# Kernel optimization log

Measured on AMD Instinct MI355X. Metric: run time of the kernel, lower is better.

## Reference

```python
import jax, jax.numpy as jnp
import numpy as np

N_NODES = 50000
N_EDGES = 800000
IN_DIM, HID, OUT = 128, 64, 64
NUM_REL = 2
LN_EPS = 1e-5


def setup_inputs() -> dict:
    key = jax.random.key(0)
    ks = jax.random.split(key, 16)
    inp = {
        "x": jax.random.normal(ks[0], (N_NODES, IN_DIM), dtype=jnp.float32),
        "edge_index": jax.random.randint(ks[1], (2, N_EDGES), 0, N_NODES, dtype=jnp.int64),
        "edge_type": jax.random.randint(ks[2], (N_EDGES,), 0, NUM_REL, dtype=jnp.int64),
        # layer 1 params (RGCNConv input->hidden + LayerNorm)
        "W1": jax.random.normal(ks[3], (NUM_REL, IN_DIM, HID), dtype=jnp.float32) * 0.05,
        "root1": jax.random.normal(ks[4], (IN_DIM, HID), dtype=jnp.float32) * 0.05,
        "b1": jnp.zeros((HID,), dtype=jnp.float32),
        "g1": jnp.ones((HID,), dtype=jnp.float32),
        "beta1": jnp.zeros((HID,), dtype=jnp.float32),
        # layer 2 params (RGCNConv hidden->output + LayerNorm)
        "W2": jax.random.normal(ks[5], (NUM_REL, HID, OUT), dtype=jnp.float32) * 0.05,
        "root2": jax.random.normal(ks[6], (HID, OUT), dtype=jnp.float32) * 0.05,
        "b2": jnp.zeros((OUT,), dtype=jnp.float32),
        "g2": jnp.ones((OUT,), dtype=jnp.float32),
        "beta2": jnp.zeros((OUT,), dtype=jnp.float32),
    }
    return inp


def rgcn_conv(x, W, root, bias, src, dst, edge_type, num_nodes):
    # PyG RGCNConv (aggr='mean'): out = x @ root + bias + sum_r mean_{j in N_r(i)} x_j @ W_r
    out = x @ root + bias
    for r in range(NUM_REL):
        mask = (edge_type == r).astype(x.dtype)        # [E]
        proj = x @ W[r]                                 # [N, out]
        msg = proj[src] * mask[:, None]                 # [E, out] gather + mask
        agg = jax.ops.segment_sum(msg, dst, num_segments=num_nodes)   # scatter-add
        cnt = jax.ops.segment_sum(mask, dst, num_segments=num_nodes)  # per-relation in-degree
        out = out + agg / jnp.maximum(cnt, 1.0)[:, None]
    return out


def layer_norm(x, g, b):
    mu = jnp.mean(x, axis=-1, keepdims=True)
    var = jnp.mean(jnp.square(x - mu), axis=-1, keepdims=True)
    return (x - mu) * jax.lax.rsqrt(var + LN_EPS) * g + b


def reference(x, edge_index, edge_type, W1, root1, b1, g1, beta1, W2, root2, b2, g2, beta2):
    src, dst = edge_index[0], edge_index[1]
    h = rgcn_conv(x, W1, root1, b1, src, dst, edge_type, x.shape[0])
    h = layer_norm(h, g1, beta1)
    h = jax.nn.gelu(h, approximate=False)  # dropout is identity in eval mode
    h = rgcn_conv(h, W2, root2, b2, src, dst, edge_type, x.shape[0])
    h = layer_norm(h, g2, beta2)
    return h
```

## Files before the change

kernel.cpp:

```cpp
#include <hip/hip_runtime.h>
#include <hip/hip_bf16.h>
#include <math.h>

#define IN_DIM 128
#define HID 64
#define NREL 2

using f32x4 = __attribute__((ext_vector_type(4))) float;
using s16x8 = __attribute__((ext_vector_type(8))) short;

__device__ __forceinline__ short f2bf(float f) {
    unsigned u = __float_as_uint(f);
    unsigned r = (u + 0x7fffu + ((u >> 16) & 1u)) >> 16;
    return (short)r;
}
__device__ __forceinline__ float bf2f(short b) {
    return __uint_as_float(((unsigned)(unsigned short)b) << 16);
}

__global__ void zero_ints(int* p, int n) {
    int i = blockIdx.x * blockDim.x + threadIdx.x;
    if (i < n) p[i] = 0;
}

__global__ void count_edges(const int* __restrict__ et, const int* __restrict__ dst,
                            int* __restrict__ cnt, int E, int N) {
    int e = blockIdx.x * blockDim.x + threadIdx.x;
    if (e < E) {
        atomicAdd(&cnt[et[e] * N + dst[e]], 1);
    }
}

#define SCAN_T 256
#define SCAN_I 4
__global__ void scan_phase1(const int* __restrict__ in, int* __restrict__ excl,
                            int* __restrict__ bsum, int n) {
    __shared__ int sdata[SCAN_T];
    int b = blockIdx.x;
    int t = threadIdx.x;
    int base = b * SCAN_T * SCAN_I;
    int v[SCAN_I];
    int s = 0;
#pragma unroll
    for (int i = 0; i < SCAN_I; ++i) {
        int idx = base + t * SCAN_I + i;
        v[i] = (idx < n) ? in[idx] : 0;
        s += v[i];
    }
    sdata[t] = s;
    __syncthreads();
    for (int off = 1; off < SCAN_T; off <<= 1) {
        int x = (t >= off) ? sdata[t - off] : 0;
        __syncthreads();
        sdata[t] += x;
        __syncthreads();
    }
    int run = sdata[t] - s;
    if (bsum && t == SCAN_T - 1) bsum[b] = sdata[SCAN_T - 1];
#pragma unroll
    for (int i = 0; i < SCAN_I; ++i) {
        int idx = base + t * SCAN_I + i;
        if (idx < n) excl[idx] = run;
        run += v[i];
    }
}

__global__ void scan_phase3(const int* __restrict__ excl, const int* __restrict__ boff,
                            int* __restrict__ rowptr, int* __restrict__ cursor,
                            int n, int total) {
    int i = blockIdx.x * blockDim.x + threadIdx.x;
    if (i < n) {
        int v = excl[i] + boff[i / (SCAN_T * SCAN_I)];
        rowptr[i] = v;
        cursor[i] = v;
    }
    if (i == 0) rowptr[n] = total;
}

__global__ void fill_edges(const int* __restrict__ et, const int* __restrict__ src,
                           const int* __restrict__ dst, int* __restrict__ cursor,
                           int* __restrict__ col, int E, int N) {
    int e = blockIdx.x * blockDim.x + threadIdx.x;
    if (e < E) {
        int slot = atomicAdd(&cursor[et[e] * N + dst[e]], 1);
        col[slot] = src[e];
    }
}

__device__ __forceinline__ void repack_one(const float* Wa, const float* Wb,
                                           const float* Wr, short* Wf, int T,
                                           int idx) {
    int g = idx >> 9;
    int r = idx & 511;
    int lane = r >> 3;
    int j = r & 7;
    int part = g & 1;
    int ct = g >> 1;
    int t = ct % T;
    int c = ct / T;
    int col = c * 16 + (lane & 15);
    int k = t * 32 + ((lane >> 4) << 3) + j;
    const float* Wg = (col < 64) ? Wa : (col < 128) ? Wb : Wr;
    float v = Wg[(size_t)k * 64 + (col & 63)];
    short hi = f2bf(v);
    Wf[idx] = part ? f2bf(v - bf2f(hi)) : hi;
}

__global__ void repack_w_frag(const float* __restrict__ W1,
                              const float* __restrict__ root1,
                              const float* __restrict__ W2,
                              const float* __restrict__ root2,
                              short* __restrict__ Wf1, short* __restrict__ Wf2) {
    const int L1 = 12 * 4 * 2 * 512;
    const int L2 = 12 * 2 * 2 * 512;
    int tid = blockIdx.x * blockDim.x + threadIdx.x;
    if (tid < L1) {
        repack_one(W1, W1 + (size_t)IN_DIM * 64, root1, Wf1, 4, tid);
    } else if (tid < L1 + L2) {
        repack_one(W2, W2 + (size_t)HID * 64, root2, Wf2, 2, tid - L1);
    }
}

template <int K>
__global__ __launch_bounds__(256) void gemm_mfma(
    const float* __restrict__ X, const short* __restrict__ Wf,
    float* __restrict__ PA, float* __restrict__ PB, float* __restrict__ PR,
    int M) {
    constexpr int T = K / 32;
    const int lane = threadIdx.x & 63;
    const int row0 = (blockIdx.x * 4 + (threadIdx.x >> 6)) * 16;

    int arow = row0 + (lane & 15);
    if (arow > M - 1) arow = M - 1;
    const float* xr = X + (size_t)arow * K + ((lane >> 4) << 3);
    const s16x8* WfV = (const s16x8*)Wf;

    f32x4 acc[12];
#pragma unroll
    for (int c = 0; c < 12; ++c) acc[c] = (f32x4){0.f, 0.f, 0.f, 0.f};

#pragma unroll
    for (int t = 0; t < T; ++t) {
        const float4 a0 = *reinterpret_cast<const float4*>(xr + t * 32);
        const float4 a1 = *reinterpret_cast<const float4*>(xr + t * 32 + 4);
        const float av[8] = {a0.x, a0.y, a0.z, a0.w, a1.x, a1.y, a1.z, a1.w};
        s16x8 ah, al;
#pragma unroll
        for (int j = 0; j < 8; ++j) {
            short h = f2bf(av[j]);
            ah[j] = h;
            al[j] = f2bf(av[j] - bf2f(h));
        }
#pragma unroll
        for (int c = 0; c < 12; ++c) {
            s16x8 bh = WfV[(size_t)((c * T + t) * 2 + 0) * 64 + lane];
            s16x8 bl = WfV[(size_t)((c * T + t) * 2 + 1) * 64 + lane];
            acc[c] = __builtin_amdgcn_mfma_f32_16x16x32_bf16(ah, bh, acc[c], 0, 0, 0);
            acc[c] = __builtin_amdgcn_mfma_f32_16x16x32_bf16(al, bh, acc[c], 0, 0, 0);
            acc[c] = __builtin_amdgcn_mfma_f32_16x16x32_bf16(ah, bl, acc[c], 0, 0, 0);
        }
    }

    const int drow = row0 + ((lane >> 4) << 2);
    const int dcol = lane & 15;
#pragma unroll
    for (int c = 0; c < 12; ++c) {
        float* base = (c < 4) ? PA : (c < 8) ? PB : PR;
        const int cc = (c & 3) * 16 + dcol;
#pragma unroll
        for (int q = 0; q < 4; ++q) {
            const int row = drow + q;
            if (row < M) base[(size_t)row * 64 + cc] = acc[c][q];
        }
    }
}

__device__ __forceinline__ float4 shfl_xor_f4(float4 v, int m) {
    return make_float4(__shfl_xor(v.x, m), __shfl_xor(v.y, m),
                       __shfl_xor(v.z, m), __shfl_xor(v.w, m));
}

__global__ __launch_bounds__(256) void agg_ln_kernel(
    const float* __restrict__ PA, const float* __restrict__ PB,
    const float* __restrict__ PR,
    const int* __restrict__ rowptr, const int* __restrict__ col,
    const float* __restrict__ bias, const float* __restrict__ g,
    const float* __restrict__ beta,
    float* __restrict__ out, int N, int gelu) {
    const int t = threadIdx.x;
    const int lane = t & 63;
    const int sub = lane >> 4;
    const int c = lane & 15;
    const int node = blockIdx.x * 4 + (t >> 6);
    if (node >= N) return;

    float4 acc = *reinterpret_cast<const float4*>(PR + (size_t)node * 64 + c * 4);
    {
        float4 b4 = *reinterpret_cast<const float4*>(bias + c * 4);
        acc.x += b4.x; acc.y += b4.y; acc.z += b4.z; acc.w += b4.w;
    }

#pragma unroll
    for (int r = 0; r < 2; ++r) {
        const float* __restrict__ P = r ? PB : PA;
        const int beg = rowptr[r * N + node];
        const int end = rowptr[r * N + node + 1];
        float4 s0 = make_float4(0.f, 0.f, 0.f, 0.f);
        float4 s1 = make_float4(0.f, 0.f, 0.f, 0.f);
        for (int i = beg + sub; i < end; i += 8) {
            const float4 v0 =
                *reinterpret_cast<const float4*>(P + (size_t)col[i] * 64 + c * 4);
            s0.x += v0.x; s0.y += v0.y; s0.z += v0.z; s0.w += v0.w;
            const int j = i + 4;
            if (j < end) {
                const float4 v1 =
                    *reinterpret_cast<const float4*>(P + (size_t)col[j] * 64 + c * 4);
                s1.x += v1.x; s1.y += v1.y; s1.z += v1.z; s1.w += v1.w;
            }
        }
        s0.x += s1.x; s0.y += s1.y; s0.z += s1.z; s0.w += s1.w;
        float4 o = shfl_xor_f4(s0, 16);
        s0.x += o.x; s0.y += o.y; s0.z += o.z; s0.w += o.w;
        o = shfl_xor_f4(s0, 32);
        s0.x += o.x; s0.y += o.y; s0.z += o.z; s0.w += o.w;
        const int deg = end - beg;
        if (deg > 0) {
            const float inv = 1.f / (float)deg;
            acc.x += s0.x * inv; acc.y += s0.y * inv;
            acc.z += s0.z * inv; acc.w += s0.w * inv;
        }
    }

    float ps = acc.x + acc.y + acc.z + acc.w;
#pragma unroll
    for (int off = 1; off <= 8; off <<= 1) ps += __shfl_xor(ps, off);
    const float mu = ps * (1.f / 64.f);
    const float4 d = make_float4(acc.x - mu, acc.y - mu, acc.z - mu, acc.w - mu);
    float vs = d.x * d.x + d.y * d.y + d.z * d.z + d.w * d.w;
#pragma unroll
    for (int off = 1; off <= 8; off <<= 1) vs += __shfl_xor(vs, off);
    const float rstd = 1.f / sqrtf(vs * (1.f / 64.f) + 1e-5f);

    const float4 g4 = *reinterpret_cast<const float4*>(g + c * 4);
    const float4 be4 = *reinterpret_cast<const float4*>(beta + c * 4);
    float4 y;
    y.x = d.x * rstd * g4.x + be4.x;
    y.y = d.y * rstd * g4.y + be4.y;
    y.z = d.z * rstd * g4.z + be4.z;
    y.w = d.w * rstd * g4.w + be4.w;

    if (gelu) {
        y.x = 0.5f * y.x * (1.f + erff(y.x * 0.70710678118654752440f));
        y.y = 0.5f * y.y * (1.f + erff(y.y * 0.70710678118654752440f));
        y.z = 0.5f * y.z * (1.f + erff(y.z * 0.70710678118654752440f));
        y.w = 0.5f * y.w * (1.f + erff(y.w * 0.70710678118654752440f));
    }

    if (sub == 0)
        *reinterpret_cast<float4*>(out + (size_t)node * 64 + c * 4) = y;
}

extern "C" void kernel_launch(void* const* d_in, const int* in_sizes, int n_in,
                              void* d_out, int out_size, void* d_ws, size_t ws_size,
                              hipStream_t stream) {
    const float* x = (const float*)d_in[0];
    const int* ei = (const int*)d_in[1];
    const int* et = (const int*)d_in[2];
    const float* W1 = (const float*)d_in[3];
    const float* root1 = (const float*)d_in[4];
    const float* b1 = (const float*)d_in[5];
    const float* g1 = (const float*)d_in[6];
    const float* beta1 = (const float*)d_in[7];
    const float* W2 = (const float*)d_in[8];
    const float* root2 = (const float*)d_in[9];
    const float* b2 = (const float*)d_in[10];
    const float* g2 = (const float*)d_in[11];
    const float* beta2 = (const float*)d_in[12];

    const int E = in_sizes[2];
    const int N = in_sizes[0] / IN_DIM;
    const int nseg = NREL * N;

    const int WF1 = 12 * 4 * 2 * 512;
    const int WF2 = 12 * 2 * 2 * 512;

    short* Wf1 = (short*)d_ws;
    short* Wf2 = Wf1 + WF1;
    float* PA = (float*)(Wf2 + WF2);
    float* PB = PA + (size_t)N * 64;
    float* PR = PB + (size_t)N * 64;
    float* H  = PR + (size_t)N * 64;
    int* cnt    = (int*)(H + (size_t)N * 64);
    int* excl   = cnt + nseg;
    int* rowptr = excl + nseg;
    int* cursor = rowptr + nseg + 1;
    int* colA   = cursor + nseg;
    int* bsum   = colA + E;
    int* boff   = bsum + 256;

    const int* esrc = ei;
    const int* edst = ei + E;

    zero_ints<<<(nseg + 255) / 256, 256, 0, stream>>>(cnt, nseg);
    count_edges<<<(E + 255) / 256, 256, 0, stream>>>(et, edst, cnt, E, N);
    int nb = (nseg + SCAN_T * SCAN_I - 1) / (SCAN_T * SCAN_I);
    scan_phase1<<<nb, SCAN_T, 0, stream>>>(cnt, excl, bsum, nseg);
    scan_phase1<<<1, SCAN_T, 0, stream>>>(bsum, boff, nullptr, nb);
    scan_phase3<<<(nseg + 255) / 256, 256, 0, stream>>>(excl, boff, rowptr, cursor,
                                                        nseg, E);
    fill_edges<<<(E + 255) / 256, 256, 0, stream>>>(et, esrc, edst, cursor, colA, E, N);

    repack_w_frag<<<(WF1 + WF2 + 255) / 256, 256, 0, stream>>>(
        W1, root1, W2, root2, Wf1, Wf2);

    int gblocks = (N + 63) / 64;
    gemm_mfma<IN_DIM><<<gblocks, 256, 0, stream>>>(x, Wf1, PA, PB, PR, N);
    agg_ln_kernel<<<(N + 3) / 4, 256, 0, stream>>>(PA, PB, PR, rowptr, colA, b1, g1,
                                                   beta1, H, N, 1);

    gemm_mfma<HID><<<gblocks, 256, 0, stream>>>(H, Wf2, PA, PB, PR, N);
    agg_ln_kernel<<<(N + 3) / 4, 256, 0, stream>>>(PA, PB, PR, rowptr, colA, b2, g2,
                                                   beta2, (float*)d_out, N, 0);
}
```

Before: 327.2 us.

## Split GEMM output columns across wave pairs and software-pipeline weight fragment loads

Each wave now computes 6 of the 12 16-column output tiles for a 16-row strip, with two waves sharing a row strip, so each block covers 32 rows and the grid doubles. A-operand loads and bf16 hi/lo splits are hoisted ahead of the MFMA loop, and B fragments are double-buffered, with the next column group loaded while the current one runs its MFMAs. This cuts accumulator registers and raises parallelism and latency hiding in the projection GEMMs. In exchange, each X row is loaded and converted twice, once per wave in the pair.

```diff
diff --git a/kernel.cpp b/kernel.cpp
--- a/kernel.cpp
+++ b/kernel.cpp
@@ -128,49 +128,86 @@
     int M) {
     constexpr int T = K / 32;
     const int lane = threadIdx.x & 63;
-    const int row0 = (blockIdx.x * 4 + (threadIdx.x >> 6)) * 16;
+    const int wid = threadIdx.x >> 6;
+    const int row0 = blockIdx.x * 32 + (wid >> 1) * 16;
+    const int cbase = (wid & 1) * 6;
 
     int arow = row0 + (lane & 15);
     if (arow > M - 1) arow = M - 1;
     const float* xr = X + (size_t)arow * K + ((lane >> 4) << 3);
     const s16x8* WfV = (const s16x8*)Wf;
 
-    f32x4 acc[12];
-#pragma unroll
-    for (int c = 0; c < 12; ++c) acc[c] = (f32x4){0.f, 0.f, 0.f, 0.f};
-
+    float4 xa[T][2];
 #pragma unroll
     for (int t = 0; t < T; ++t) {
-        const float4 a0 = *reinterpret_cast<const float4*>(xr + t * 32);
-        const float4 a1 = *reinterpret_cast<const float4*>(xr + t * 32 + 4);
-        const float av[8] = {a0.x, a0.y, a0.z, a0.w, a1.x, a1.y, a1.z, a1.w};
-        s16x8 ah, al;
+        xa[t][0] = *reinterpret_cast<const float4*>(xr + t * 32);
+        xa[t][1] = *reinterpret_cast<const float4*>(xr + t * 32 + 4);
+    }
+    s16x8 ah[T], al[T];
+#pragma unroll
+    for (int t = 0; t < T; ++t) {
+        const float av[8] = {xa[t][0].x, xa[t][0].y, xa[t][0].z, xa[t][0].w,
+                             xa[t][1].x, xa[t][1].y, xa[t][1].z, xa[t][1].w};
 #pragma unroll
         for (int j = 0; j < 8; ++j) {
             short h = f2bf(av[j]);
-            ah[j] = h;
-            al[j] = f2bf(av[j] - bf2f(h));
+            ah[t][j] = h;
+            al[t][j] = f2bf(av[j] - bf2f(h));
         }
-#pragma unroll
-        for (int c = 0; c < 12; ++c) {
-            s16x8 bh = WfV[(size_t)((c * T + t) * 2 + 0) * 64 + lane];
-            s16x8 bl = WfV[(size_t)((c * T + t) * 2 + 1) * 64 + lane];
-            acc[c] = __builtin_amdgcn_mfma_f32_16x16x32_bf16(ah, bh, acc[c], 0, 0, 0);
-            acc[c] = __builtin_amdgcn_mfma_f32_16x16x32_bf16(al, bh, acc[c], 0, 0, 0);
-            acc[c] = __builtin_amdgcn_mfma_f32_16x16x32_bf16(ah, bl, acc[c], 0, 0, 0);
-        }
-    }
+    }
+
+    f32x4 acc[6];
+#pragma unroll
+    for (int c = 0; c < 6; ++c) acc[c] = (f32x4){0.f, 0.f, 0.f, 0.f};
+
+    s16x8 bhA[T], blA[T], bhB[T], blB[T];
+
+#define LOADB(H, L, CG)                                                       \
+    {                                                                         \
+        _Pragma("unroll") for (int t = 0; t < T; ++t) {                       \
+            H[t] = WfV[(size_t)(((CG) * T + t) * 2 + 0) * 64 + lane];         \
+            L[t] = WfV[(size_t)(((CG) * T + t) * 2 + 1) * 64 + lane];         \
+        }                                                                     \
+    }
+#define DOMFMA(H, L, CI)                                                      \
+    {                                                                         \
+        _Pragma("unroll") for (int t = 0; t < T; ++t) {                       \
+            acc[CI] = __builtin_amdgcn_mfma_f32_16x16x32_bf16(ah[t], H[t],    \
+                                                              acc[CI], 0, 0, 0); \
+            acc[CI] = __builtin_amdgcn_mfma_f32_16x16x32_bf16(al[t], H[t],    \
+                                                              acc[CI], 0, 0, 0); \
+            acc[CI] = __builtin_amdgcn_mfma_f32_16x16x32_bf16(ah[t], L[t],    \
+                                                              acc[CI], 0, 0, 0); \
+        }                                                                     \
+    }
+
+    LOADB(bhA, blA, cbase + 0);
+    LOADB(bhB, blB, cbase + 1);
+    DOMFMA(bhA, blA, 0);
+    LOADB(bhA, blA, cbase + 2);
+    DOMFMA(bhB, blB, 1);
+    LOADB(bhB, blB, cbase + 3);
+    DOMFMA(bhA, blA, 2);
+    LOADB(bhA, blA, cbase + 4);
+    DOMFMA(bhB, blB, 3);
+    LOADB(bhB, blB, cbase + 5);
+    DOMFMA(bhA, blA, 4);
+    DOMFMA(bhB, blB, 5);
+
+#undef LOADB
+#undef DOMFMA
 
     const int drow = row0 + ((lane >> 4) << 2);
     const int dcol = lane & 15;
 #pragma unroll
-    for (int c = 0; c < 12; ++c) {
-        float* base = (c < 4) ? PA : (c < 8) ? PB : PR;
-        const int cc = (c & 3) * 16 + dcol;
+    for (int ci = 0; ci < 6; ++ci) {
+        const int cg = cbase + ci;
+        float* base = (cg < 4) ? PA : (cg < 8) ? PB : PR;
+        const int cc = (cg & 3) * 16 + dcol;
 #pragma unroll
         for (int q = 0; q < 4; ++q) {
             const int row = drow + q;
-            if (row < M) base[(size_t)row * 64 + cc] = acc[c][q];
+            if (row < M) base[(size_t)row * 64 + cc] = acc[ci][q];
         }
     }
 }
@@ -313,7 +350,7 @@
     repack_w_frag<<<(WF1 + WF2 + 255) / 256, 256, 0, stream>>>(
         W1, root1, W2, root2, Wf1, Wf2);
 
-    int gblocks = (N + 63) / 64;
+    int gblocks = (N + 31) / 32;
     gemm_mfma<IN_DIM><<<gblocks, 256, 0, stream>>>(x, Wf1, PA, PB, PR, N);
     agg_ln_kernel<<<(N + 3) / 4, 256, 0, stream>>>(PA, PB, PR, rowptr, colA, b1, g1,
                                                    beta1, H, N, 1);
```

New measurement: 298.4 us. -8.8%, faster.
